# Kernel tuning notes

Measured on AMD Instinct MI355X. Metric: run time of the kernel, lower is better.

The kernel has to match this reference:

```python
import jax, jax.numpy as jnp
import numpy as np

C = 256          # channels
NH = 8           # heads
DH = 64          # dim_head
NMEM = 4         # num_mem_kv
HIDDEN = NH * DH # 512
SCALE = DH ** (-0.5)


def _rmsnorm(x, gain):
    # F.normalize(x, dim=1) * gain * sqrt(C)  (scale-only RMS norm over channel dim)
    n = jnp.sqrt(jnp.sum(x * x, axis=1, keepdims=True))
    return x / jnp.maximum(n, 1e-12) * gain * (x.shape[1] ** 0.5)


def setup_inputs() -> dict:
    key = jax.random.key(0)
    ks = jax.random.split(key, 6)
    B, Hh, Ww = 16, 64, 64
    return {
        "x": jax.random.normal(ks[0], (B, C, Hh, Ww), jnp.float32),
        "gain1": jnp.ones((1, C, 1, 1), jnp.float32),
        "w_qkv": jax.random.normal(ks[1], (3 * HIDDEN, C), jnp.float32) * 0.02,
        "mem_kv": jax.random.normal(ks[2], (2, NH, DH, NMEM), jnp.float32),
        "w_out": jax.random.normal(ks[3], (C, HIDDEN), jnp.float32) * 0.02,
        "b_out": jnp.zeros((C,), jnp.float32),
        "gain2": jnp.ones((1, C, 1, 1), jnp.float32),
    }


def reference(x, gain1, w_qkv, mem_kv, w_out, b_out, gain2):
    B, _, Hh, Ww = x.shape
    N = Hh * Ww
    # pre-norm
    xn = _rmsnorm(x, gain1)
    # 1x1 conv QKV projection (no bias) == channel GEMM
    qkv = jnp.einsum('oc,bchw->bohw', w_qkv, xn)          # [B, 3*hidden, H, W]
    qkv = qkv.reshape(B, 3, NH, DH, N)                    # chunk + 'b (h c) x y -> b h c (x y)'
    q, k, v = qkv[:, 0], qkv[:, 1], qkv[:, 2]             # [B, h, d, N]
    # learned global memory kv, broadcast over batch
    mem_k = jnp.broadcast_to(mem_kv[0], (B, NH, DH, NMEM))
    mem_v = jnp.broadcast_to(mem_kv[1], (B, NH, DH, NMEM))
    k = jnp.concatenate([mem_k, k], axis=-1)              # [B, h, d, NMEM+N]
    v = jnp.concatenate([mem_v, v], axis=-1)
    # dual softmax: q over feature dim d, k over token dim n
    q = jax.nn.softmax(q, axis=-2) * SCALE
    k = jax.nn.softmax(k, axis=-1)
    # linear attention: O(N) context
    context = jnp.einsum('bhdn,bhen->bhde', k, v)         # [B, h, d, e]
    out = jnp.einsum('bhde,bhdn->bhen', context, q)       # [B, h, e, N]
    out = out.reshape(B, HIDDEN, Hh, Ww)
    # 1x1 conv out projection (with bias) + post RMSNorm
    out = jnp.einsum('oc,bchw->bohw', w_out, out) + b_out[None, :, None, None]
    return _rmsnorm(out, gain2)
```

## Files before the change

kernel.cpp:

```cpp
#include <hip/hip_runtime.h>

typedef __attribute__((ext_vector_type(8))) short bf16x8;
typedef __attribute__((ext_vector_type(4))) short bf16x4;
typedef __attribute__((ext_vector_type(4))) float f32x4;
typedef unsigned short u16;

constexpr int B_   = 16;
constexpr int C_   = 256;
constexpr int NH   = 8;
constexpr int DH   = 64;
constexpr int NMEM = 4;
constexpr int HID  = 512;
constexpr int QKVC = 1536;
constexpr int N_   = 4096;
constexpr int CTXS = 4224;

__device__ __forceinline__ u16 f2b(float f) {
  union { float f; unsigned u; } v{f};
  unsigned r = v.u + 0x7fff + ((v.u >> 16) & 1);
  return (u16)(r >> 16);
}
__device__ __forceinline__ float b2f(u16 h) {
  union { unsigned u; float f; } v; v.u = ((unsigned)h) << 16; return v.f;
}

__device__ __forceinline__ void gld_lds16(const u16* g, u16* l) {
  __builtin_amdgcn_global_load_lds(
      (const __attribute__((address_space(1))) unsigned*)g,
      (__attribute__((address_space(3))) unsigned*)l, 16, 0, 0);
}

__global__ void k_cvtw(const float* __restrict__ wq, const float* __restrict__ wo,
                       u16* __restrict__ wqb, u16* __restrict__ wob) {
  int i = blockIdx.x * 256 + threadIdx.x;
  for (int idx = i; idx < QKVC * C_; idx += gridDim.x * 256) wqb[idx] = f2b(wq[idx]);
  for (int idx = i; idx < C_ * HID; idx += gridDim.x * 256) wob[idx] = f2b(wo[idx]);
}

__global__ __launch_bounds__(256) void k_rms1(const float* __restrict__ x,
                                              const float* __restrict__ g1,
                                              u16* __restrict__ xbT) {
  int g = blockIdx.y;
  int n = blockIdx.x * 64 + (threadIdx.x & 63);
  int ch = threadIdx.x >> 6;
  __shared__ float ssp[4][64];
  __shared__ float invs[64];
  const float* xp = x + (size_t)g * C_ * N_ + n;
  float ss = 0.f;
  #pragma unroll 16
  for (int c = ch * 64; c < ch * 64 + 64; ++c) {
    float v = xp[(size_t)c * N_];
    ss += v * v;
  }
  ssp[ch][n & 63] = ss;
  __syncthreads();
  if (threadIdx.x < 64) {
    float tot = (ssp[0][threadIdx.x] + ssp[1][threadIdx.x]) +
                (ssp[2][threadIdx.x] + ssp[3][threadIdx.x]);
    invs[threadIdx.x] = 16.0f / fmaxf(sqrtf(tot), 1e-12f);
  }
  __syncthreads();
  float inv = invs[n & 63];
  u16* op = xbT + ((size_t)g * N_ + n) * C_;
  #pragma unroll 2
  for (int c0 = ch * 64; c0 < ch * 64 + 64; c0 += 8) {
    union { bf16x8 v; u16 u[8]; } pk;
    #pragma unroll
    for (int j = 0; j < 8; ++j) pk.u[j] = f2b(xp[(size_t)(c0 + j) * N_] * inv * g1[c0 + j]);
    *(bf16x8*)(op + c0) = pk.v;
  }
}

__global__ __launch_bounds__(256) void k_kvctx(const u16* __restrict__ Wb,
                                               const u16* __restrict__ XT,
                                               float* __restrict__ ctxp) {
  __shared__ __align__(16) u16 smem[16384];
  u16* Ws = smem;
  u16* Xs = smem + 8192;
  u16* Pl = smem;
  u16* Vl = smem + 8192;

  int cpx = gridDim.x >> 3;
  int bid = blockIdx.x;
  int L = (bid & 7) * cpx + (bid >> 3);
  int h = L & 7, nc = (L >> 3) & 7, g = L >> 6;
  int t = threadIdx.x, wave = t >> 6, lane = t & 63;
  int wm = wave >> 1, wn = wave & 1;
  int kg = lane >> 4, lr = lane & 15;

  const u16* WK = Wb + (size_t)(HID + h * DH) * C_;
  const u16* WV = Wb + (size_t)(2 * HID + h * DH) * C_;
  const u16* Xg = XT + ((size_t)g * N_ + nc * 512) * C_;

  int rl8 = lane >> 3;
  int cs8 = (lane & 7) ^ rl8;
  const u16* Wsrc = (wave < 2) ? WK : WV;

  f32x4 acc2[4];
  #pragma unroll
  for (int nf = 0; nf < 4; ++nf) acc2[nf] = (f32x4)0.f;
  float rs[4] = {0.f, 0.f, 0.f, 0.f};

  for (int it = 0; it < 4; ++it) {
    f32x4 acc[4][4];
    #pragma unroll
    for (int i = 0; i < 4; ++i)
      #pragma unroll
      for (int j = 0; j < 4; ++j) acc[i][j] = (f32x4)0.f;

    for (int k0 = 0; k0 < C_; k0 += 64) {
      #pragma unroll
      for (int q = 0; q < 4; ++q) {
        int rb = wave * 32 + q * 8;
        int rw = (rb & 63) + rl8;
        int rx = it * 128 + rb + rl8;
        gld_lds16(Wsrc + (size_t)rw * C_ + k0 + cs8 * 8, Ws + rb * 64);
        gld_lds16(Xg + (size_t)rx * C_ + k0 + cs8 * 8, Xs + rb * 64);
      }
      __syncthreads();
      #pragma unroll
      for (int ks = 0; ks < 2; ++ks) {
        int ch = ks * 4 + kg;
        bf16x8 a[4], bv[4];
        #pragma unroll
        for (int mf = 0; mf < 4; ++mf) {
          int r = wm * 64 + mf * 16 + lr;
          a[mf] = *(const bf16x8*)(Xs + r * 64 + ((ch ^ (r & 7)) * 8));
        }
        #pragma unroll
        for (int nf = 0; nf < 4; ++nf) {
          int r = wn * 64 + nf * 16 + lr;
          bv[nf] = *(const bf16x8*)(Ws + r * 64 + ((ch ^ (r & 7)) * 8));
        }
        #pragma unroll
        for (int mf = 0; mf < 4; ++mf)
          #pragma unroll
          for (int nf = 0; nf < 4; ++nf)
            acc[mf][nf] = __builtin_amdgcn_mfma_f32_16x16x32_bf16(a[mf], bv[nf], acc[mf][nf], 0, 0, 0);
      }
      __syncthreads();
    }

    if (wn == 0) {
      #pragma unroll
      for (int mf = 0; mf < 4; ++mf) {
        int nb = wm * 64 + mf * 16 + kg * 4;
        int cc = nb >> 3, off = nb & 7;
        #pragma unroll
        for (int nf = 0; nf < 4; ++nf) {
          int d = nf * 16 + lr;
          float e0 = __expf(acc[mf][nf][0]);
          float e1 = __expf(acc[mf][nf][1]);
          float e2 = __expf(acc[mf][nf][2]);
          float e3 = __expf(acc[mf][nf][3]);
          rs[nf] += (e0 + e1) + (e2 + e3);
          union { bf16x4 v; u16 u[4]; } pk;
          pk.u[0] = f2b(e0); pk.u[1] = f2b(e1); pk.u[2] = f2b(e2); pk.u[3] = f2b(e3);
          *(bf16x4*)(Pl + d * 128 + ((cc ^ (d & 15)) * 8) + off) = pk.v;
        }
      }
    } else {
      #pragma unroll
      for (int mf = 0; mf < 4; ++mf) {
        int nb = wm * 64 + mf * 16 + kg * 4;
        int cc = nb >> 3, off = nb & 7;
        #pragma unroll
        for (int nf = 0; nf < 4; ++nf) {
          int e = nf * 16 + lr;
          union { bf16x4 v; u16 u[4]; } pk;
          pk.u[0] = f2b(acc[mf][nf][0]); pk.u[1] = f2b(acc[mf][nf][1]);
          pk.u[2] = f2b(acc[mf][nf][2]); pk.u[3] = f2b(acc[mf][nf][3]);
          *(bf16x4*)(Vl + e * 128 + ((cc ^ (e & 15)) * 8) + off) = pk.v;
        }
      }
    }
    __syncthreads();

    #pragma unroll
    for (int k = 0; k < 4; ++k) {
      int c = k * 4 + kg;
      bf16x8 af = *(const bf16x8*)(Pl + (wave * 16 + lr) * 128 + ((c ^ lr) * 8));
      #pragma unroll
      for (int nf = 0; nf < 4; ++nf) {
        bf16x8 bfv = *(const bf16x8*)(Vl + (nf * 16 + lr) * 128 + ((c ^ lr) * 8));
        acc2[nf] = __builtin_amdgcn_mfma_f32_16x16x32_bf16(af, bfv, acc2[nf], 0, 0, 0);
      }
    }
    __syncthreads();
  }

  float* cgp = ctxp + ((size_t)(g * NH + h) * 8 + nc) * CTXS;
  #pragma unroll
  for (int nf = 0; nf < 4; ++nf)
    #pragma unroll
    for (int j = 0; j < 4; ++j) {
      int d = wave * 16 + kg * 4 + j;
      int e = nf * 16 + lr;
      cgp[d * 64 + e] = acc2[nf][j];
    }
  if (wn == 0) {
    #pragma unroll
    for (int nf = 0; nf < 4; ++nf) {
      rs[nf] += __shfl_xor(rs[nf], 16);
      rs[nf] += __shfl_xor(rs[nf], 32);
    }
    if (lane < 16) {
      #pragma unroll
      for (int nf = 0; nf < 4; ++nf)
        cgp[4096 + wm * 64 + nf * 16 + lane] = rs[nf];
    }
  }
}

__global__ __launch_bounds__(256) void k_cfin(const float* __restrict__ ctxp,
                                              const float* __restrict__ memkv,
                                              u16* __restrict__ ctxTb) {
  int g = blockIdx.y, h = blockIdx.x;
  int t = threadIdx.x;
  __shared__ float emk[DH * NMEM];
  __shared__ float sd[DH];
  const float* mk = memkv + (size_t)h * DH * NMEM;
  const float* mv = memkv + (size_t)(NH + h) * DH * NMEM;
  const float* cp = ctxp + (size_t)(g * NH + h) * 8 * CTXS;
  emk[t] = __expf(mk[t]);
  __syncthreads();
  if (t < DH) {
    float s = 0.f;
    #pragma unroll
    for (int p = 0; p < 8; ++p)
      s += cp[p * CTXS + 4096 + t] + cp[p * CTXS + 4160 + t];
    #pragma unroll
    for (int j = 0; j < NMEM; ++j) s += emk[t * 4 + j];
    sd[t] = s;
  }
  __syncthreads();
  u16* ct = ctxTb + (size_t)(g * NH + h) * 4096;
  #pragma unroll
  for (int i = 0; i < 16; ++i) {
    int idx = t + 256 * i;
    int d = idx >> 6, e = idx & 63;
    float v = 0.f;
    #pragma unroll
    for (int p = 0; p < 8; ++p) v += cp[p * CTXS + idx];
    #pragma unroll
    for (int j = 0; j < NMEM; ++j) v += emk[d * 4 + j] * mv[e * 4 + j];
    ct[e * 64 + d] = f2b(v / sd[d]);
  }
}

__global__ __launch_bounds__(256) void k_qpv(const u16* __restrict__ Wq,
                                             const u16* __restrict__ XT,
                                             const u16* __restrict__ ctxTb,
                                             u16* __restrict__ attnT) {
  __shared__ __align__(16) u16 smem[24576];
  u16* Ws = smem;
  u16* Xs = smem + 8192;
  u16* cl = smem + 16384;

  int cpx = gridDim.x >> 3;
  int bid = blockIdx.x;
  int L = (bid & 7) * cpx + (bid >> 3);
  int hh = L & 3, rest = L >> 2;
  int nc = rest & 31, g = rest >> 5;
  int t = threadIdx.x, wave = t >> 6, lane = t & 63;
  int wm = wave >> 1, wn = wave & 1;
  int kg = lane >> 4, lr = lane & 15;

  {
    const u16* cg = ctxTb + (size_t)(g * NH + hh * 2) * 4096;
    #pragma unroll
    for (int i = 0; i < 4; ++i) {
      int id = t + 256 * i;
      int r = id >> 3, c = id & 7;
      *(bf16x8*)(cl + (r >> 6) * 4096 + (r & 63) * 64 + ((c ^ (r & 7)) * 8)) =
          *(const bf16x8*)(cg + id * 8);
    }
  }

  const u16* Ag = Wq + (size_t)(hh * 128) * C_;
  const u16* Bg = XT + ((size_t)g * N_ + nc * 128) * C_;
  int rl8 = lane >> 3;
  int cs8 = (lane & 7) ^ rl8;

  f32x4 acc[4][4];
  #pragma unroll
  for (int i = 0; i < 4; ++i)
    #pragma unroll
    for (int j = 0; j < 4; ++j) acc[i][j] = (f32x4)0.f;

  for (int k0 = 0; k0 < C_; k0 += 64) {
    #pragma unroll
    for (int q = 0; q < 4; ++q) {
      int rb = wave * 32 + q * 8;
      gld_lds16(Ag + (size_t)(rb + rl8) * C_ + k0 + cs8 * 8, Ws + rb * 64);
      gld_lds16(Bg + (size_t)(rb + rl8) * C_ + k0 + cs8 * 8, Xs + rb * 64);
    }
    __syncthreads();
    #pragma unroll
    for (int ks = 0; ks < 2; ++ks) {
      int ch = ks * 4 + kg;
      bf16x8 a[4], bv[4];
      #pragma unroll
      for (int mf = 0; mf < 4; ++mf) {
        int r = wm * 64 + mf * 16 + lr;
        a[mf] = *(const bf16x8*)(Ws + r * 64 + ((ch ^ (r & 7)) * 8));
      }
      #pragma unroll
      for (int nf = 0; nf < 4; ++nf) {
        int r = wn * 64 + nf * 16 + lr;
        bv[nf] = *(const bf16x8*)(Xs + r * 64 + ((ch ^ (r & 7)) * 8));
      }
      #pragma unroll
      for (int mf = 0; mf < 4; ++mf)
        #pragma unroll
        for (int nf = 0; nf < 4; ++nf)
          acc[mf][nf] = __builtin_amdgcn_mfma_f32_16x16x32_bf16(a[mf], bv[nf], acc[mf][nf], 0, 0, 0);
    }
    __syncthreads();
  }

  float colsum[4];
  #pragma unroll
  for (int nf = 0; nf < 4; ++nf) {
    float s = 0.f;
    #pragma unroll
    for (int mf = 0; mf < 4; ++mf)
      #pragma unroll
      for (int j = 0; j < 4; ++j) {
        float e = __expf(acc[mf][nf][j]);
        acc[mf][nf][j] = e;
        s += e;
      }
    colsum[nf] = s;
  }
  #pragma unroll
  for (int nf = 0; nf < 4; ++nf) {
    colsum[nf] += __shfl_xor(colsum[nf], 16);
    colsum[nf] += __shfl_xor(colsum[nf], 32);
  }
  u16* qh = smem + wm * 8192;
  #pragma unroll
  for (int nf = 0; nf < 4; ++nf) {
    float invs = 0.125f / colsum[nf];
    int n = wn * 64 + nf * 16 + lr;
    #pragma unroll
    for (int mf = 0; mf < 4; ++mf)
      #pragma unroll
      for (int jp = 0; jp < 2; ++jp) {
        int d0 = mf * 16 + kg * 4 + jp * 2;
        u16 lo = f2b(acc[mf][nf][jp * 2] * invs);
        u16 hi = f2b(acc[mf][nf][jp * 2 + 1] * invs);
        unsigned pk = (unsigned)lo | ((unsigned)hi << 16);
        int idx = n * 64 + (((d0 >> 3) ^ (n & 7)) * 8) + (d0 & 7);
        *(unsigned*)(qh + idx) = pk;
      }
  }
  __syncthreads();

  int hcl = wave >> 1, nh2 = wave & 1;
  const u16* qh2 = smem + hcl * 8192;
  const u16* clh = cl + hcl * 4096;
  f32x4 acc2[4][4];
  #pragma unroll
  for (int i = 0; i < 4; ++i)
    #pragma unroll
    for (int j = 0; j < 4; ++j) acc2[i][j] = (f32x4)0.f;

  #pragma unroll
  for (int kk = 0; kk < 2; ++kk) {
    int c = kk * 4 + kg;
    bf16x8 a2[4], b2[4];
    #pragma unroll
    for (int mf = 0; mf < 4; ++mf) {
      int rn = nh2 * 64 + mf * 16 + lr;
      a2[mf] = *(const bf16x8*)(qh2 + rn * 64 + ((c ^ (rn & 7)) * 8));
    }
    #pragma unroll
    for (int nf = 0; nf < 4; ++nf) {
      int re = nf * 16 + lr;
      b2[nf] = *(const bf16x8*)(clh + re * 64 + ((c ^ (re & 7)) * 8));
    }
    #pragma unroll
    for (int mf = 0; mf < 4; ++mf)
      #pragma unroll
      for (int nf = 0; nf < 4; ++nf)
        acc2[mf][nf] = __builtin_amdgcn_mfma_f32_16x16x32_bf16(a2[mf], b2[nf], acc2[mf][nf], 0, 0, 0);
  }

  int h = hh * 2 + hcl;
  u16* op = attnT + ((size_t)g * N_ + nc * 128) * HID + h * 64;
  #pragma unroll
  for (int mf = 0; mf < 4; ++mf)
    #pragma unroll
    for (int nf = 0; nf < 4; ++nf)
      #pragma unroll
      for (int j = 0; j < 4; ++j) {
        int n = nh2 * 64 + mf * 16 + kg * 4 + j;
        int e = nf * 16 + lr;
        op[(size_t)n * HID + e] = f2b(acc2[mf][nf][j]);
      }
}

__global__ __launch_bounds__(256) void k_out(const u16* __restrict__ Wb,
                                             const u16* __restrict__ AT,
                                             const float* __restrict__ bias,
                                             const float* __restrict__ g2,
                                             float* __restrict__ out) {
  constexpr int BN = 128;
  __shared__ __align__(16) u16 As[256 * 64];
  __shared__ __align__(16) u16 Bs[BN * 64];
  __shared__ float part[4][BN];
  int g  = blockIdx.y;
  int n0 = blockIdx.x * BN;
  int t = threadIdx.x, wave = t >> 6, lane = t & 63;
  int kg = lane >> 4, lr = lane & 15;

  const u16* Bg = AT + ((size_t)g * N_ + n0) * HID;

  int rl8 = lane >> 3;
  int cs8 = (lane & 7) ^ rl8;

  f32x4 acc[4][8];
  #pragma unroll
  for (int i = 0; i < 4; ++i)
    #pragma unroll
    for (int j = 0; j < 8; ++j) acc[i][j] = (f32x4)0.f;

  for (int k0 = 0; k0 < HID; k0 += 64) {
    #pragma unroll
    for (int q = 0; q < 8; ++q) {
      int rb = wave * 64 + q * 8;
      gld_lds16(Wb + (size_t)(rb + rl8) * HID + k0 + cs8 * 8, As + rb * 64);
    }
    #pragma unroll
    for (int q = 0; q < 4; ++q) {
      int rb = wave * 32 + q * 8;
      gld_lds16(Bg + (size_t)(rb + rl8) * HID + k0 + cs8 * 8, Bs + rb * 64);
    }
    __syncthreads();
    #pragma unroll
    for (int ks = 0; ks < 2; ++ks) {
      int ch = ks * 4 + kg;
      bf16x8 a[4], bv[8];
      #pragma unroll
      for (int mf = 0; mf < 4; ++mf) {
        int r = wave * 64 + mf * 16 + lr;
        a[mf] = *(const bf16x8*)(As + r * 64 + ((ch ^ (r & 7)) * 8));
      }
      #pragma unroll
      for (int nf = 0; nf < 8; ++nf) {
        int r = nf * 16 + lr;
        bv[nf] = *(const bf16x8*)(Bs + r * 64 + ((ch ^ (r & 7)) * 8));
      }
      #pragma unroll
      for (int mf = 0; mf < 4; ++mf)
        #pragma unroll
        for (int nf = 0; nf < 8; ++nf)
          acc[mf][nf] = __builtin_amdgcn_mfma_f32_16x16x32_bf16(a[mf], bv[nf], acc[mf][nf], 0, 0, 0);
    }
    __syncthreads();
  }
  float colsq[8] = {0.f, 0.f, 0.f, 0.f, 0.f, 0.f, 0.f, 0.f};
  #pragma unroll
  for (int mf = 0; mf < 4; ++mf)
    #pragma unroll
    for (int j = 0; j < 4; ++j) {
      int row = wave * 64 + mf * 16 + kg * 4 + j;
      float bs = bias[row];
      #pragma unroll
      for (int nf = 0; nf < 8; ++nf) {
        float v = acc[mf][nf][j] + bs;
        acc[mf][nf][j] = v;
        colsq[nf] += v * v;
      }
    }
  #pragma unroll
  for (int nf = 0; nf < 8; ++nf) {
    colsq[nf] += __shfl_xor(colsq[nf], 16);
    colsq[nf] += __shfl_xor(colsq[nf], 32);
  }
  if (kg == 0) {
    #pragma unroll
    for (int nf = 0; nf < 8; ++nf) part[wave][nf * 16 + lr] = colsq[nf];
  }
  __syncthreads();
  float* og = out + (size_t)g * C_ * N_ + n0;
  #pragma unroll
  for (int nf = 0; nf < 8; ++nf) {
    int col = nf * 16 + lr;
    float tot = part[0][col] + part[1][col] + part[2][col] + part[3][col];
    float invn = 16.0f / fmaxf(sqrtf(tot), 1e-12f);
    #pragma unroll
    for (int mf = 0; mf < 4; ++mf)
      #pragma unroll
      for (int j = 0; j < 4; ++j) {
        int row = wave * 64 + mf * 16 + kg * 4 + j;
        og[(size_t)row * N_ + col] = acc[mf][nf][j] * invn * g2[row];
      }
  }
}

extern "C" void kernel_launch(void* const* d_in, const int* in_sizes, int n_in,
                              void* d_out, int out_size, void* d_ws, size_t ws_size,
                              hipStream_t stream) {
  (void)in_sizes; (void)n_in; (void)out_size;
  const float* x      = (const float*)d_in[0];
  const float* gain1  = (const float*)d_in[1];
  const float* w_qkv  = (const float*)d_in[2];
  const float* mem_kv = (const float*)d_in[3];
  const float* w_out  = (const float*)d_in[4];
  const float* b_out  = (const float*)d_in[5];
  const float* gain2  = (const float*)d_in[6];
  float* out = (float*)d_out;

  char* ws = (char*)d_ws;
  u16* wqkvb = (u16*)ws;
  u16* woutb = (u16*)(ws + 786432);
  size_t shared_b = 1048576;

  const size_t xbT_b   = (size_t)N_ * C_ * 2;
  const size_t attnT_b = (size_t)HID * N_ * 2;
  const size_t ctxp_b  = (size_t)NH * 8 * CTXS * 4;
  const size_t ctxT_b  = (size_t)NH * 4096 * 2;
  const size_t per_b   = xbT_b + attnT_b + ctxp_b + ctxT_b;

  int G = 16;
  while (G > 1 && shared_b + (size_t)G * per_b > ws_size) G >>= 1;

  char* base = ws + shared_b;
  u16*   xbT   = (u16*)base;
  u16*   attnT = (u16*)(base + (size_t)G * xbT_b);
  float* ctxp  = (float*)(base + (size_t)G * (xbT_b + attnT_b));
  u16*   ctxTb = (u16*)(base + (size_t)G * (xbT_b + attnT_b + ctxp_b));

  k_cvtw<<<256, 256, 0, stream>>>(w_qkv, w_out, wqkvb, woutb);

  for (int b0 = 0; b0 < B_; b0 += G) {
    const float* xc = x + (size_t)b0 * C_ * N_;
    float*       oc = out + (size_t)b0 * C_ * N_;
    k_rms1  <<<dim3(N_ / 64, G),   256, 0, stream>>>(xc, gain1, xbT);
    k_kvctx <<<dim3(64 * G),       256, 0, stream>>>(wqkvb, xbT, ctxp);
    k_cfin  <<<dim3(NH, G),        256, 0, stream>>>(ctxp, mem_kv, ctxTb);
    k_qpv   <<<dim3(4 * 32 * G),   256, 0, stream>>>(wqkvb, xbT, ctxTb, attnT);
    k_out   <<<dim3(N_ / 128, G),  256, 0, stream>>>(woutb, attnT, b_out, gain2, oc);
  }
}
```

Baseline: 175.5 us.

## Double-buffer K/V context GEMM tiles with async LDS prefetch

Doubles the shared memory in k_kvctx so W and X tiles sit in two ping-pong buffers. The global-to-LDS load for the next k-step is issued before computing the current one, which overlaps load latency with MFMA work. __syncthreads is replaced by inline-asm barriers that wait only on the counters needed, and the P and V buffers get their own region. The larger LDS footprint can lower occupancy, and removing the barrier after each k-step relies on the single wait at the top of the next step to avoid overwriting data still being read.

```diff
diff --git a/kernel.cpp b/kernel.cpp
--- a/kernel.cpp
+++ b/kernel.cpp
@@ -14,6 +14,9 @@
 constexpr int QKVC = 1536;
 constexpr int N_   = 4096;
 constexpr int CTXS = 4224;
+
+#define KBAR() asm volatile("s_waitcnt vmcnt(0) lgkmcnt(0)\ns_barrier" ::: "memory")
+#define SBAR() asm volatile("s_waitcnt lgkmcnt(0)\ns_barrier" ::: "memory")
 
 __device__ __forceinline__ u16 f2b(float f) {
   union { float f; unsigned u; } v{f};
@@ -74,11 +77,9 @@
 __global__ __launch_bounds__(256) void k_kvctx(const u16* __restrict__ Wb,
                                                const u16* __restrict__ XT,
                                                float* __restrict__ ctxp) {
-  __shared__ __align__(16) u16 smem[16384];
-  u16* Ws = smem;
-  u16* Xs = smem + 8192;
-  u16* Pl = smem;
-  u16* Vl = smem + 8192;
+  __shared__ __align__(16) u16 smem[32768];
+  u16* Pl = smem + 16384;
+  u16* Vl = smem + 24576;
 
   int cpx = gridDim.x >> 3;
   int bid = blockIdx.x;
@@ -96,11 +97,27 @@
   int cs8 = (lane & 7) ^ rl8;
   const u16* Wsrc = (wave < 2) ? WK : WV;
 
+  auto STAGE = [&](int j) {
+    int it_ = j >> 2, k0_ = (j & 3) * 64;
+    u16* Wd = smem + (j & 1) * 16384;
+    u16* Xd = Wd + 8192;
+    #pragma unroll
+    for (int q = 0; q < 4; ++q) {
+      int rb = wave * 32 + q * 8;
+      int rw = (rb & 63) + rl8;
+      int rx = it_ * 128 + rb + rl8;
+      gld_lds16(Wsrc + (size_t)rw * C_ + k0_ + cs8 * 8, Wd + rb * 64);
+      gld_lds16(Xg + (size_t)rx * C_ + k0_ + cs8 * 8, Xd + rb * 64);
+    }
+  };
+
   f32x4 acc2[4];
   #pragma unroll
   for (int nf = 0; nf < 4; ++nf) acc2[nf] = (f32x4)0.f;
   float rs[4] = {0.f, 0.f, 0.f, 0.f};
 
+  STAGE(0);
+
   for (int it = 0; it < 4; ++it) {
     f32x4 acc[4][4];
     #pragma unroll
@@ -108,16 +125,12 @@
       #pragma unroll
       for (int j = 0; j < 4; ++j) acc[i][j] = (f32x4)0.f;
 
-    for (int k0 = 0; k0 < C_; k0 += 64) {
-      #pragma unroll
-      for (int q = 0; q < 4; ++q) {
-        int rb = wave * 32 + q * 8;
-        int rw = (rb & 63) + rl8;
-        int rx = it * 128 + rb + rl8;
-        gld_lds16(Wsrc + (size_t)rw * C_ + k0 + cs8 * 8, Ws + rb * 64);
-        gld_lds16(Xg + (size_t)rx * C_ + k0 + cs8 * 8, Xs + rb * 64);
-      }
-      __syncthreads();
+    for (int k0i = 0; k0i < 4; ++k0i) {
+      int j = it * 4 + k0i;
+      KBAR();
+      if (j + 1 < 16) STAGE(j + 1);
+      u16* Wc = smem + (j & 1) * 16384;
+      u16* Xc = Wc + 8192;
       #pragma unroll
       for (int ks = 0; ks < 2; ++ks) {
         int ch = ks * 4 + kg;
@@ -125,12 +138,12 @@
         #pragma unroll
         for (int mf = 0; mf < 4; ++mf) {
           int r = wm * 64 + mf * 16 + lr;
-          a[mf] = *(const bf16x8*)(Xs + r * 64 + ((ch ^ (r & 7)) * 8));
+          a[mf] = *(const bf16x8*)(Xc + r * 64 + ((ch ^ (r & 7)) * 8));
         }
         #pragma unroll
         for (int nf = 0; nf < 4; ++nf) {
           int r = wn * 64 + nf * 16 + lr;
-          bv[nf] = *(const bf16x8*)(Ws + r * 64 + ((ch ^ (r & 7)) * 8));
+          bv[nf] = *(const bf16x8*)(Wc + r * 64 + ((ch ^ (r & 7)) * 8));
         }
         #pragma unroll
         for (int mf = 0; mf < 4; ++mf)
@@ -138,8 +151,8 @@
           for (int nf = 0; nf < 4; ++nf)
             acc[mf][nf] = __builtin_amdgcn_mfma_f32_16x16x32_bf16(a[mf], bv[nf], acc[mf][nf], 0, 0, 0);
       }
-      __syncthreads();
-    }
+    }
+    SBAR();
 
     if (wn == 0) {
       #pragma unroll
@@ -174,7 +187,7 @@
         }
       }
     }
-    __syncthreads();
+    SBAR();
 
     #pragma unroll
     for (int k = 0; k < 4; ++k) {
@@ -186,7 +199,7 @@
         acc2[nf] = __builtin_amdgcn_mfma_f32_16x16x32_bf16(af, bfv, acc2[nf], 0, 0, 0);
       }
     }
-    __syncthreads();
+    SBAR();
   }
 
   float* cgp = ctxp + ((size_t)(g * NH + h) * 8 + nc) * CTXS;
```

Result: slower. 184.9 us (+5.4%).

## Fold attention context into output projection weights and fuse Q-proj with out-proj

Applied to the files above, without the earlier changes.

The per-head context matrix is now pre-multiplied into the output projection weights per batch (k_cwo), producing a combined 256x512 weight. A single fused kernel then computes the Q projection, the feature softmax and the output projection with bias and post-RMSNorm, with no attnT intermediate written to or read from global memory. This removes a kernel launch and a large bf16 round trip. In exchange it adds a small per-batch GEMM, more shared-memory reuse with extra barriers, and 512-thread blocks.

```diff
diff --git a/kernel.cpp b/kernel.cpp
--- a/kernel.cpp
+++ b/kernel.cpp
@@ -212,13 +212,19 @@
   }
 }
 
-__global__ __launch_bounds__(256) void k_cfin(const float* __restrict__ ctxp,
-                                              const float* __restrict__ memkv,
-                                              u16* __restrict__ ctxTb) {
+__global__ __launch_bounds__(256) void k_cwo(const float* __restrict__ ctxp,
+                                             const float* __restrict__ memkv,
+                                             const u16* __restrict__ Wo,
+                                             u16* __restrict__ wo2) {
   int g = blockIdx.y, h = blockIdx.x;
-  int t = threadIdx.x;
+  int t = threadIdx.x, wave = t >> 6, lane = t & 63;
+  int kg = lane >> 4, lr = lane & 15;
+  int rl8 = lane >> 3, cs8 = (lane & 7) ^ rl8;
   __shared__ float emk[DH * NMEM];
   __shared__ float sd[DH];
+  __shared__ __align__(16) u16 Cl[64 * 64];
+  __shared__ __align__(16) u16 As2[256 * 64];
+
   const float* mk = memkv + (size_t)h * DH * NMEM;
   const float* mv = memkv + (size_t)(NH + h) * DH * NMEM;
   const float* cp = ctxp + (size_t)(g * NH + h) * 8 * CTXS;
@@ -233,8 +239,12 @@
     for (int j = 0; j < NMEM; ++j) s += emk[t * 4 + j];
     sd[t] = s;
   }
+  #pragma unroll
+  for (int q = 0; q < 8; ++q) {
+    int rb = wave * 64 + q * 8;
+    gld_lds16(Wo + (size_t)(rb + rl8) * HID + h * DH + cs8 * 8, As2 + rb * 64);
+  }
   __syncthreads();
-  u16* ct = ctxTb + (size_t)(g * NH + h) * 4096;
   #pragma unroll
   for (int i = 0; i < 16; ++i) {
     int idx = t + 256 * i;
@@ -244,43 +254,80 @@
     for (int p = 0; p < 8; ++p) v += cp[p * CTXS + idx];
     #pragma unroll
     for (int j = 0; j < NMEM; ++j) v += emk[d * 4 + j] * mv[e * 4 + j];
-    ct[e * 64 + d] = f2b(v / sd[d]);
-  }
-}
-
-__global__ __launch_bounds__(256) void k_qpv(const u16* __restrict__ Wq,
-                                             const u16* __restrict__ XT,
-                                             const u16* __restrict__ ctxTb,
-                                             u16* __restrict__ attnT) {
-  __shared__ __align__(16) u16 smem[24576];
-  u16* Ws = smem;
-  u16* Xs = smem + 8192;
-  u16* cl = smem + 16384;
+    Cl[d * 64 + (((e >> 3) ^ (d & 7)) * 8) + (e & 7)] = f2b(v / sd[d]);
+  }
+  __syncthreads();
+  f32x4 acc[4][4];
+  #pragma unroll
+  for (int i = 0; i < 4; ++i)
+    #pragma unroll
+    for (int j = 0; j < 4; ++j) acc[i][j] = (f32x4)0.f;
+  #pragma unroll
+  for (int ks = 0; ks < 2; ++ks) {
+    int ch = ks * 4 + kg;
+    bf16x8 a[4], b[4];
+    #pragma unroll
+    for (int mf = 0; mf < 4; ++mf) {
+      int r = wave * 64 + mf * 16 + lr;
+      a[mf] = *(const bf16x8*)(As2 + r * 64 + ((ch ^ (r & 7)) * 8));
+    }
+    #pragma unroll
+    for (int nf = 0; nf < 4; ++nf) {
+      int rd = nf * 16 + lr;
+      b[nf] = *(const bf16x8*)(Cl + rd * 64 + ((ch ^ (rd & 7)) * 8));
+    }
+    #pragma unroll
+    for (int mf = 0; mf < 4; ++mf)
+      #pragma unroll
+      for (int nf = 0; nf < 4; ++nf)
+        acc[mf][nf] = __builtin_amdgcn_mfma_f32_16x16x32_bf16(a[mf], b[nf], acc[mf][nf], 0, 0, 0);
+  }
+  u16* og = wo2 + (size_t)g * 256 * 512;
+  #pragma unroll
+  for (int mf = 0; mf < 4; ++mf)
+    #pragma unroll
+    for (int nf = 0; nf < 4; ++nf)
+      #pragma unroll
+      for (int j = 0; j < 4; ++j) {
+        int c = wave * 64 + mf * 16 + kg * 4 + j;
+        int dd = nf * 16 + lr;
+        og[(size_t)c * 512 + h * DH + dd] = f2b(acc[mf][nf][j]);
+      }
+}
+
+__global__ __launch_bounds__(512) void k_qout(const u16* __restrict__ Wq,
+                                              const u16* __restrict__ XT,
+                                              const u16* __restrict__ Wo2,
+                                              const float* __restrict__ bias,
+                                              const float* __restrict__ g2,
+                                              float* __restrict__ out) {
+  __shared__ __align__(16) u16 smem[32768];
+  u16* R0 = smem;
+  u16* R1 = smem + 16384;
 
   int cpx = gridDim.x >> 3;
   int bid = blockIdx.x;
   int L = (bid & 7) * cpx + (bid >> 3);
-  int hh = L & 3, rest = L >> 2;
-  int nc = rest & 31, g = rest >> 5;
+  int nc = L & 63, g = L >> 6;
   int t = threadIdx.x, wave = t >> 6, lane = t & 63;
-  int wm = wave >> 1, wn = wave & 1;
   int kg = lane >> 4, lr = lane & 15;
+  int rl4 = lane >> 2, cs4 = (lane & 3) ^ (rl4 & 3);
+  int rl8 = lane >> 3, cs8 = (lane & 7) ^ rl8;
+
+  const u16* Xg = XT + ((size_t)g * N_ + nc * 64) * C_;
+  const u16* W2g = Wo2 + (size_t)g * 256 * 512;
 
   {
-    const u16* cg = ctxTb + (size_t)(g * NH + hh * 2) * 4096;
-    #pragma unroll
-    for (int i = 0; i < 4; ++i) {
-      int id = t + 256 * i;
-      int r = id >> 3, c = id & 7;
-      *(bf16x8*)(cl + (r >> 6) * 4096 + (r & 63) * 64 + ((c ^ (r & 7)) * 8)) =
-          *(const bf16x8*)(cg + id * 8);
-    }
-  }
-
-  const u16* Ag = Wq + (size_t)(hh * 128) * C_;
-  const u16* Bg = XT + ((size_t)g * N_ + nc * 128) * C_;
-  int rl8 = lane >> 3;
-  int cs8 = (lane & 7) ^ rl8;
+    int xrow_off = lane >> 5;
+    int c32 = lane & 31;
+    #pragma unroll
+    for (int q = 0; q < 4; ++q) {
+      int base = wave * 8 + q * 2;
+      int row = base + xrow_off;
+      int sw = (c32 & 24) | ((c32 & 7) ^ (row & 7));
+      gld_lds16(Xg + (size_t)row * C_ + sw * 8, R1 + base * 256);
+    }
+  }
 
   f32x4 acc[4][4];
   #pragma unroll
@@ -288,34 +335,32 @@
     #pragma unroll
     for (int j = 0; j < 4; ++j) acc[i][j] = (f32x4)0.f;
 
-  for (int k0 = 0; k0 < C_; k0 += 64) {
+  for (int k0i = 0; k0i < 8; ++k0i) {
+    int k0 = k0i * 32;
     #pragma unroll
     for (int q = 0; q < 4; ++q) {
-      int rb = wave * 32 + q * 8;
-      gld_lds16(Ag + (size_t)(rb + rl8) * C_ + k0 + cs8 * 8, Ws + rb * 64);
-      gld_lds16(Bg + (size_t)(rb + rl8) * C_ + k0 + cs8 * 8, Xs + rb * 64);
+      int rb = ((wave * 4 + q) & 31) * 16;
+      gld_lds16(Wq + (size_t)(rb + rl4) * C_ + k0 + cs4 * 8, R0 + rb * 32);
     }
     __syncthreads();
-    #pragma unroll
-    for (int ks = 0; ks < 2; ++ks) {
-      int ch = ks * 4 + kg;
-      bf16x8 a[4], bv[4];
-      #pragma unroll
-      for (int mf = 0; mf < 4; ++mf) {
-        int r = wm * 64 + mf * 16 + lr;
-        a[mf] = *(const bf16x8*)(Ws + r * 64 + ((ch ^ (r & 7)) * 8));
-      }
-      #pragma unroll
-      for (int nf = 0; nf < 4; ++nf) {
-        int r = wn * 64 + nf * 16 + lr;
-        bv[nf] = *(const bf16x8*)(Xs + r * 64 + ((ch ^ (r & 7)) * 8));
-      }
-      #pragma unroll
-      for (int mf = 0; mf < 4; ++mf)
-        #pragma unroll
-        for (int nf = 0; nf < 4; ++nf)
-          acc[mf][nf] = __builtin_amdgcn_mfma_f32_16x16x32_bf16(a[mf], bv[nf], acc[mf][nf], 0, 0, 0);
-    }
+    bf16x8 a[4], bv[4];
+    #pragma unroll
+    for (int mf = 0; mf < 4; ++mf) {
+      int r = wave * 64 + mf * 16 + lr;
+      a[mf] = *(const bf16x8*)(R0 + r * 32 + ((kg ^ (r & 3)) * 8));
+    }
+    #pragma unroll
+    for (int nf = 0; nf < 4; ++nf) {
+      int bn = nf * 16 + lr;
+      int c32 = k0i * 4 + kg;
+      int sw = (c32 & 24) | ((c32 & 7) ^ (bn & 7));
+      bv[nf] = *(const bf16x8*)(R1 + bn * 256 + sw * 8);
+    }
+    #pragma unroll
+    for (int mf = 0; mf < 4; ++mf)
+      #pragma unroll
+      for (int nf = 0; nf < 4; ++nf)
+        acc[mf][nf] = __builtin_amdgcn_mfma_f32_16x16x32_bf16(a[mf], bv[nf], acc[mf][nf], 0, 0, 0);
     __syncthreads();
   }
 
@@ -337,165 +382,110 @@
   for (int nf = 0; nf < 4; ++nf) {
     colsum[nf] += __shfl_xor(colsum[nf], 16);
     colsum[nf] += __shfl_xor(colsum[nf], 32);
-  }
-  u16* qh = smem + wm * 8192;
+    colsum[nf] = 0.125f / colsum[nf];
+  }
+
+  f32x4 acc2[2][4];
+  #pragma unroll
+  for (int i = 0; i < 2; ++i)
+    #pragma unroll
+    for (int j = 0; j < 4; ++j) acc2[i][j] = (f32x4)0.f;
+
+  #pragma unroll
+  for (int half = 0; half < 2; ++half) {
+    if ((wave >> 2) == half) {
+      #pragma unroll
+      for (int nf = 0; nf < 4; ++nf) {
+        int n = nf * 16 + lr;
+        float invs = colsum[nf];
+        #pragma unroll
+        for (int mf = 0; mf < 4; ++mf)
+          #pragma unroll
+          for (int jp = 0; jp < 2; ++jp) {
+            int oc = (wave & 3) * 64 + mf * 16 + kg * 4 + jp * 2;
+            u16 lo = f2b(acc[mf][nf][jp * 2] * invs);
+            u16 hi = f2b(acc[mf][nf][jp * 2 + 1] * invs);
+            unsigned pk = (unsigned)lo | ((unsigned)hi << 16);
+            int c8 = oc >> 3;
+            int sw = (c8 & 24) | ((c8 & 7) ^ (n & 7));
+            *(unsigned*)(R1 + n * 256 + sw * 8 + (oc & 7)) = pk;
+          }
+      }
+    }
+    __syncthreads();
+    for (int k0l = 0; k0l < 4; ++k0l) {
+      int cb = half * 256 + k0l * 64;
+      #pragma unroll
+      for (int q = 0; q < 4; ++q) {
+        int rb = ((wave * 4 + q) & 31) * 8;
+        gld_lds16(W2g + (size_t)(rb + rl8) * 512 + cb + cs8 * 8, R0 + rb * 64);
+      }
+      __syncthreads();
+      #pragma unroll
+      for (int ks = 0; ks < 2; ++ks) {
+        int ch = ks * 4 + kg;
+        bf16x8 a2[2], b2[4];
+        #pragma unroll
+        for (int mf = 0; mf < 2; ++mf) {
+          int r = wave * 32 + mf * 16 + lr;
+          a2[mf] = *(const bf16x8*)(R0 + r * 64 + ((ch ^ (r & 7)) * 8));
+        }
+        #pragma unroll
+        for (int nf = 0; nf < 4; ++nf) {
+          int bn = nf * 16 + lr;
+          int c8 = k0l * 8 + ks * 4 + kg;
+          int sw = (c8 & 24) | ((c8 & 7) ^ (bn & 7));
+          b2[nf] = *(const bf16x8*)(R1 + bn * 256 + sw * 8);
+        }
+        #pragma unroll
+        for (int mf = 0; mf < 2; ++mf)
+          #pragma unroll
+          for (int nf = 0; nf < 4; ++nf)
+            acc2[mf][nf] = __builtin_amdgcn_mfma_f32_16x16x32_bf16(a2[mf], b2[nf], acc2[mf][nf], 0, 0, 0);
+      }
+      __syncthreads();
+    }
+  }
+
+  float colsq[4] = {0.f, 0.f, 0.f, 0.f};
+  #pragma unroll
+  for (int mf = 0; mf < 2; ++mf)
+    #pragma unroll
+    for (int j = 0; j < 4; ++j) {
+      int c = wave * 32 + mf * 16 + kg * 4 + j;
+      float bs = bias[c];
+      #pragma unroll
+      for (int nf = 0; nf < 4; ++nf) {
+        float v = acc2[mf][nf][j] + bs;
+        acc2[mf][nf][j] = v;
+        colsq[nf] += v * v;
+      }
+    }
   #pragma unroll
   for (int nf = 0; nf < 4; ++nf) {
-    float invs = 0.125f / colsum[nf];
-    int n = wn * 64 + nf * 16 + lr;
-    #pragma unroll
-    for (int mf = 0; mf < 4; ++mf)
-      #pragma unroll
-      for (int jp = 0; jp < 2; ++jp) {
-        int d0 = mf * 16 + kg * 4 + jp * 2;
-        u16 lo = f2b(acc[mf][nf][jp * 2] * invs);
-        u16 hi = f2b(acc[mf][nf][jp * 2 + 1] * invs);
-        unsigned pk = (unsigned)lo | ((unsigned)hi << 16);
-        int idx = n * 64 + (((d0 >> 3) ^ (n & 7)) * 8) + (d0 & 7);
-        *(unsigned*)(qh + idx) = pk;
-      }
-  }
-  __syncthreads();
-
-  int hcl = wave >> 1, nh2 = wave & 1;
-  const u16* qh2 = smem + hcl * 8192;
-  const u16* clh = cl + hcl * 4096;
-  f32x4 acc2[4][4];
-  #pragma unroll
-  for (int i = 0; i < 4; ++i)
-    #pragma unroll
-    for (int j = 0; j < 4; ++j) acc2[i][j] = (f32x4)0.f;
-
-  #pragma unroll
-  for (int kk = 0; kk < 2; ++kk) {
-    int c = kk * 4 + kg;
-    bf16x8 a2[4], b2[4];
-    #pragma unroll
-    for (int mf = 0; mf < 4; ++mf) {
-      int rn = nh2 * 64 + mf * 16 + lr;
-      a2[mf] = *(const bf16x8*)(qh2 + rn * 64 + ((c ^ (rn & 7)) * 8));
-    }
-    #pragma unroll
-    for (int nf = 0; nf < 4; ++nf) {
-      int re = nf * 16 + lr;
-      b2[nf] = *(const bf16x8*)(clh + re * 64 + ((c ^ (re & 7)) * 8));
-    }
-    #pragma unroll
-    for (int mf = 0; mf < 4; ++mf)
-      #pragma unroll
-      for (int nf = 0; nf < 4; ++nf)
-        acc2[mf][nf] = __builtin_amdgcn_mfma_f32_16x16x32_bf16(a2[mf], b2[nf], acc2[mf][nf], 0, 0, 0);
-  }
-
-  int h = hh * 2 + hcl;
-  u16* op = attnT + ((size_t)g * N_ + nc * 128) * HID + h * 64;
-  #pragma unroll
-  for (int mf = 0; mf < 4; ++mf)
-    #pragma unroll
-    for (int nf = 0; nf < 4; ++nf)
-      #pragma unroll
-      for (int j = 0; j < 4; ++j) {
-        int n = nh2 * 64 + mf * 16 + kg * 4 + j;
-        int e = nf * 16 + lr;
-        op[(size_t)n * HID + e] = f2b(acc2[mf][nf][j]);
-      }
-}
-
-__global__ __launch_bounds__(256) void k_out(const u16* __restrict__ Wb,
-                                             const u16* __restrict__ AT,
-                                             const float* __restrict__ bias,
-                                             const float* __restrict__ g2,
-                                             float* __restrict__ out) {
-  constexpr int BN = 128;
-  __shared__ __align__(16) u16 As[256 * 64];
-  __shared__ __align__(16) u16 Bs[BN * 64];
-  __shared__ float part[4][BN];
-  int g  = blockIdx.y;
-  int n0 = blockIdx.x * BN;
-  int t = threadIdx.x, wave = t >> 6, lane = t & 63;
-  int kg = lane >> 4, lr = lane & 15;
-
-  const u16* Bg = AT + ((size_t)g * N_ + n0) * HID;
-
-  int rl8 = lane >> 3;
-  int cs8 = (lane & 7) ^ rl8;
-
-  f32x4 acc[4][8];
-  #pragma unroll
-  for (int i = 0; i < 4; ++i)
-    #pragma unroll
-    for (int j = 0; j < 8; ++j) acc[i][j] = (f32x4)0.f;
-
-  for (int k0 = 0; k0 < HID; k0 += 64) {
-    #pragma unroll
-    for (int q = 0; q < 8; ++q) {
-      int rb = wave * 64 + q * 8;
-      gld_lds16(Wb + (size_t)(rb + rl8) * HID + k0 + cs8 * 8, As + rb * 64);
-    }
-    #pragma unroll
-    for (int q = 0; q < 4; ++q) {
-      int rb = wave * 32 + q * 8;
-      gld_lds16(Bg + (size_t)(rb + rl8) * HID + k0 + cs8 * 8, Bs + rb * 64);
-    }
-    __syncthreads();
-    #pragma unroll
-    for (int ks = 0; ks < 2; ++ks) {
-      int ch = ks * 4 + kg;
-      bf16x8 a[4], bv[8];
-      #pragma unroll
-      for (int mf = 0; mf < 4; ++mf) {
-        int r = wave * 64 + mf * 16 + lr;
-        a[mf] = *(const bf16x8*)(As + r * 64 + ((ch ^ (r & 7)) * 8));
-      }
-      #pragma unroll
-      for (int nf = 0; nf < 8; ++nf) {
-        int r = nf * 16 + lr;
-        bv[nf] = *(const bf16x8*)(Bs + r * 64 + ((ch ^ (r & 7)) * 8));
-      }
-      #pragma unroll
-      for (int mf = 0; mf < 4; ++mf)
-        #pragma unroll
-        for (int nf = 0; nf < 8; ++nf)
-          acc[mf][nf] = __builtin_amdgcn_mfma_f32_16x16x32_bf16(a[mf], bv[nf], acc[mf][nf], 0, 0, 0);
-    }
-    __syncthreads();
-  }
-  float colsq[8] = {0.f, 0.f, 0.f, 0.f, 0.f, 0.f, 0.f, 0.f};
-  #pragma unroll
-  for (int mf = 0; mf < 4; ++mf)
-    #pragma unroll
-    for (int j = 0; j < 4; ++j) {
-      int row = wave * 64 + mf * 16 + kg * 4 + j;
-      float bs = bias[row];
-      #pragma unroll
-      for (int nf = 0; nf < 8; ++nf) {
-        float v = acc[mf][nf][j] + bs;
-        acc[mf][nf][j] = v;
-        colsq[nf] += v * v;
-      }
-    }
-  #pragma unroll
-  for (int nf = 0; nf < 8; ++nf) {
     colsq[nf] += __shfl_xor(colsq[nf], 16);
     colsq[nf] += __shfl_xor(colsq[nf], 32);
   }
+  float* part = (float*)R0;
   if (kg == 0) {
     #pragma unroll
-    for (int nf = 0; nf < 8; ++nf) part[wave][nf * 16 + lr] = colsq[nf];
+    for (int nf = 0; nf < 4; ++nf) part[wave * 64 + nf * 16 + lr] = colsq[nf];
   }
   __syncthreads();
-  float* og = out + (size_t)g * C_ * N_ + n0;
-  #pragma unroll
-  for (int nf = 0; nf < 8; ++nf) {
+  float* og = out + (size_t)g * C_ * N_ + nc * 64;
+  #pragma unroll
+  for (int nf = 0; nf < 4; ++nf) {
     int col = nf * 16 + lr;
-    float tot = part[0][col] + part[1][col] + part[2][col] + part[3][col];
+    float tot = 0.f;
+    #pragma unroll
+    for (int w = 0; w < 8; ++w) tot += part[w * 64 + col];
     float invn = 16.0f / fmaxf(sqrtf(tot), 1e-12f);
     #pragma unroll
-    for (int mf = 0; mf < 4; ++mf)
+    for (int mf = 0; mf < 2; ++mf)
       #pragma unroll
       for (int j = 0; j < 4; ++j) {
-        int row = wave * 64 + mf * 16 + kg * 4 + j;
-        og[(size_t)row * N_ + col] = acc[mf][nf][j] * invn * g2[row];
+        int c = wave * 32 + mf * 16 + kg * 4 + j;
+        og[(size_t)c * N_ + col] = acc2[mf][nf][j] * invn * g2[c];
       }
   }
 }
@@ -518,20 +508,18 @@
   u16* woutb = (u16*)(ws + 786432);
   size_t shared_b = 1048576;
 
-  const size_t xbT_b   = (size_t)N_ * C_ * 2;
-  const size_t attnT_b = (size_t)HID * N_ * 2;
-  const size_t ctxp_b  = (size_t)NH * 8 * CTXS * 4;
-  const size_t ctxT_b  = (size_t)NH * 4096 * 2;
-  const size_t per_b   = xbT_b + attnT_b + ctxp_b + ctxT_b;
+  const size_t xbT_b  = (size_t)N_ * C_ * 2;
+  const size_t ctxp_b = (size_t)NH * 8 * CTXS * 4;
+  const size_t wo2_b  = (size_t)256 * 512 * 2;
+  const size_t per_b  = xbT_b + ctxp_b + wo2_b;
 
   int G = 16;
   while (G > 1 && shared_b + (size_t)G * per_b > ws_size) G >>= 1;
 
   char* base = ws + shared_b;
-  u16*   xbT   = (u16*)base;
-  u16*   attnT = (u16*)(base + (size_t)G * xbT_b);
-  float* ctxp  = (float*)(base + (size_t)G * (xbT_b + attnT_b));
-  u16*   ctxTb = (u16*)(base + (size_t)G * (xbT_b + attnT_b + ctxp_b));
+  u16*   xbT  = (u16*)base;
+  float* ctxp = (float*)(base + (size_t)G * xbT_b);
+  u16*   wo2  = (u16*)(base + (size_t)G * (xbT_b + ctxp_b));
 
   k_cvtw<<<256, 256, 0, stream>>>(w_qkv, w_out, wqkvb, woutb);
 
@@ -540,8 +528,7 @@
     float*       oc = out + (size_t)b0 * C_ * N_;
     k_rms1  <<<dim3(N_ / 64, G),   256, 0, stream>>>(xc, gain1, xbT);
     k_kvctx <<<dim3(64 * G),       256, 0, stream>>>(wqkvb, xbT, ctxp);
-    k_cfin  <<<dim3(NH, G),        256, 0, stream>>>(ctxp, mem_kv, ctxTb);
-    k_qpv   <<<dim3(4 * 32 * G),   256, 0, stream>>>(wqkvb, xbT, ctxTb, attnT);
-    k_out   <<<dim3(N_ / 128, G),  256, 0, stream>>>(woutb, attnT, b_out, gain2, oc);
-  }
-}
+    k_cwo   <<<dim3(NH, G),        256, 0, stream>>>(ctxp, mem_kv, woutb, wo2);
+    k_qout  <<<dim3(64 * G),       512, 0, stream>>>(wqkvb, xbT, wo2, b_out, gain2, oc);
+  }
+}
```

Result: faster. 172.1 us (-2.0%).
